# Performance work log

Hardware: AMD Instinct MI355X
Metric: run time of the kernel (lower is better)

The kernel has to match this reference:

```python
import jax, jax.numpy as jnp
import numpy as np


def _conv(x, w, b, pad):
    y = jax.lax.conv_general_dilated(x, w, (1, 1), [(pad, pad), (pad, pad)],
                                     dimension_numbers=('NCHW', 'OIHW', 'NCHW'))
    return y + b[None, :, None, None]


def _pool(x):
    return jax.lax.reduce_window(x, -jnp.inf, jax.lax.max, (1, 1, 2, 2), (1, 1, 2, 2), 'VALID')


def _up(x):
    return jnp.repeat(jnp.repeat(x, 2, axis=2), 2, axis=3)


def _unet(x, p):
    r = jax.nn.relu
    e1 = r(_conv(x, p['enc1_w'], p['enc1_b'], 1))                            # [B,16,H,W]
    e2 = r(_conv(_pool(e1), p['enc2_w'], p['enc2_b'], 1))                    # [B,32,H/2,W/2]
    bt = r(_conv(_pool(e2), p['bott_w'], p['bott_b'], 1))                    # [B,64,H/4,W/4]
    d2 = r(_conv(jnp.concatenate([_up(bt), e2], 1), p['dec2_w'], p['dec2_b'], 1))
    d1 = r(_conv(jnp.concatenate([_up(d2), e1], 1), p['dec1_w'], p['dec1_b'], 1))
    return _conv(d1, p['out_w'], p['out_b'], 0)                              # [B,C,H,W]


def _global_match(ref_e, cur_e):
    # FEELVOS global matching: for each current-frame pixel, distance to the
    # nearest reference-frame pixel in embedding space, mapped through
    # d = 1 - 2/(1+exp(||e_p - e_q||^2)). Monotone, so apply after the min.
    N, E, H, W = ref_e.shape
    a = ref_e.reshape(N, E, H * W).transpose(0, 2, 1)   # [N, P, E] reference pixels
    b = cur_e.reshape(N, E, H * W).transpose(0, 2, 1)   # [N, Q, E] current pixels
    d2 = (jnp.sum(a * a, -1)[:, :, None] + jnp.sum(b * b, -1)[:, None, :]
          - 2.0 * jnp.einsum('npe,nqe->npq', a, b))     # [N, P, Q]
    dmin = jnp.min(jnp.maximum(d2, 0.0), axis=1)        # [N, Q] nearest-neighbor dist^2
    return (1.0 - 2.0 * jax.nn.sigmoid(-dmin)).reshape(N, 1, H, W)


def setup_inputs() -> dict:
    key = jax.random.key(0)
    ks = jax.random.split(key, 16)
    B, C, H, W, CIN = 2, 4, 48, 48, 3

    def w(k, shape):
        fan_in = int(np.prod(shape[1:]))
        return jax.random.normal(k, shape, jnp.float32) * np.float32(1.0 / np.sqrt(fan_in))

    return {
        'x1': jax.random.uniform(ks[0], (B, C, H, W), jnp.float32),
        'x2': jax.random.uniform(ks[1], (B, C, H, W), jnp.float32),
        'x3': jax.random.normal(ks[2], (B, CIN, H, W), jnp.float32),
        'enc1_w': w(ks[3], (16, CIN, 3, 3)), 'enc1_b': jnp.zeros((16,), jnp.float32),
        'enc2_w': w(ks[4], (32, 16, 3, 3)), 'enc2_b': jnp.zeros((32,), jnp.float32),
        'bott_w': w(ks[5], (64, 32, 3, 3)), 'bott_b': jnp.zeros((64,), jnp.float32),
        'dec2_w': w(ks[6], (32, 96, 3, 3)), 'dec2_b': jnp.zeros((32,), jnp.float32),
        'dec1_w': w(ks[7], (16, 48, 3, 3)), 'dec1_b': jnp.zeros((16,), jnp.float32),
        'out_w': w(ks[8], (C, 16, 1, 1)), 'out_b': jnp.zeros((C,), jnp.float32),
        'emb_w': w(ks[9], (100, 1, 3, 3)), 'emb_b': jnp.zeros((100,), jnp.float32),
        'dsh_w': w(ks[10], (1, C + 3, 3, 3)), 'dsh_b': jnp.zeros((1,), jnp.float32),
    }


def reference(x1, x2, x3, enc1_w, enc1_b, enc2_w, enc2_b, bott_w, bott_b,
              dec2_w, dec2_b, dec1_w, dec1_b, out_w, out_b, emb_w, emb_b,
              dsh_w, dsh_b):
    p = dict(enc1_w=enc1_w, enc1_b=enc1_b, enc2_w=enc2_w, enc2_b=enc2_b,
             bott_w=bott_w, bott_b=bott_b, dec2_w=dec2_w, dec2_b=dec2_b,
             dec1_w=dec1_w, dec1_b=dec1_b, out_w=out_w, out_b=out_b)
    B, C, H, W = x1.shape
    x3s = _unet(x3, p)                        # backbone on current frame -> [B,C,H,W]
    # fold the per-class Python loop into the batch axis (shared weights)
    x1f = x1.reshape(B * C, 1, H, W)
    x2f = x2.reshape(B * C, 1, H, W)
    x3f = x3s.reshape(B * C, 1, H, W)
    e1 = _conv(x1f, emb_w, emb_b, 1)          # [B*C,100,H,W]
    e2 = _conv(x2f, emb_w, emb_b, 1)
    e3 = _conv(x3f, emb_w, emb_b, 1)
    gm = _global_match(e1, e3)                # first-frame matching  [B*C,1,H,W]
    lm = _global_match(e2, e3)                # previous-frame matching
    x3rep = jnp.broadcast_to(x3s[:, None], (B, C, C, H, W)).reshape(B * C, C, H, W)
    x_t = jnp.concatenate([x3rep, gm, lm, x2f], axis=1)   # [B*C, C+3, H, W]
    logits = _conv(x_t, dsh_w, dsh_b, 1).reshape(B, C, H, W)
    # faithful to the original final loop: output is cat(logits[C-2], logits[C-1])
    return jnp.concatenate([logits[:, C - 2:C - 1], logits[:, C - 1:C]], axis=1)
```

## Files before the change

kernel.cpp:

```cpp
#include <hip/hip_runtime.h>
#include <math.h>

#define THREADS 256
#define HW 2304

typedef __attribute__((ext_vector_type(8))) short short8;
typedef __attribute__((ext_vector_type(4))) float f32x4;
typedef __attribute__((ext_vector_type(8))) unsigned short us8;

typedef const __attribute__((address_space(1))) void* gas_p;
typedef __attribute__((address_space(3))) void* las_p;

__device__ __forceinline__ void gll16(const void* g, const void* l) {
    __builtin_amdgcn_global_load_lds((gas_p)g, (las_p)l, 16, 0, 0);
}

__device__ __forceinline__ void stage_rows(const float* __restrict__ src, float* __restrict__ dst,
                                           int nch, int chStride, int H, int W,
                                           int rlo, int rcount, int tid, int nthr, bool relu) {
    int rowfl = W + 4;
    int total = nch * rcount * rowfl;
    float4 z = make_float4(0.f, 0.f, 0.f, 0.f);
    for (int i = tid; i * 4 < total; i += nthr) ((float4*)dst)[i] = z;
    __syncthreads();
    int w2 = W >> 1;
    int m = nch * rcount * w2;
    for (int i = tid; i < m; i += nthr) {
        int c2 = i % w2;
        int rr = (i / w2) % rcount;
        int ch = i / (w2 * rcount);
        int srow = rlo + rr;
        if (srow < 0 || srow >= H) continue;
        float2 v = *(const float2*)(src + (size_t)ch * chStride + srow * W + 2 * c2);
        if (relu) { v.x = fmaxf(v.x, 0.f); v.y = fmaxf(v.y, 0.f); }
        *(float2*)(dst + (size_t)ch * rcount * rowfl + rr * rowfl + 2 + 2 * c2) = v;
    }
    __syncthreads();
}

#define LOAD_W9(wlbase, ci)                                        \
    const float4* wp4 = (const float4*)((wlbase) + (ci) * 12);     \
    float4 wa = wp4[0], wb = wp4[1], wc = wp4[2];                  \
    const float w9[9] = {wa.x, wa.y, wa.z, wa.w, wb.x, wb.y, wb.z, wb.w, wc.x};

__device__ __forceinline__ void emb_body(const float* __restrict__ src, int arr, int ni, int pt,
                                         const float* __restrict__ ew, const float* __restrict__ eb,
                                         unsigned short* __restrict__ hl, float* __restrict__ nrm,
                                         float* wl, int tid, int nthr) {
    for (int i = tid; i < 900; i += nthr) wl[(i / 9) * 12 + (i % 9)] = ew[i];
    for (int i = tid; i < 100; i += nthr) wl[1200 + i] = eb[i];
    __syncthreads();

    int pix = pt * 256 + tid;
    int x = pix % 48, y = pix / 48;
    float p9[9];
    #pragma unroll
    for (int ky = 0; ky < 3; ++ky)
        #pragma unroll
        for (int kx = 0; kx < 3; ++kx) {
            int yy = y + ky - 1, xx = x + kx - 1;
            p9[ky * 3 + kx] = (yy >= 0 && yy < 48 && xx >= 0 && xx < 48) ? src[yy * 48 + xx] : 0.f;
        }

    float nsum = 0.f;
    char* rowp = (char*)(hl + (((size_t)(arr * 4 + ni)) * HW + pix) * 256);
    for (int g = 0; g < 16; ++g) {
        us8 vh, vl;
        #pragma unroll
        for (int j = 0; j < 8; ++j) {
            int e = g * 8 + j;
            float v = 0.f;
            if (e < 100) {
                v = wl[1200 + e];
                #pragma unroll
                for (int k = 0; k < 9; ++k) v = fmaf(p9[k], wl[e * 12 + k], v);
                nsum = fmaf(v, v, nsum);
            }
            unsigned bits = __float_as_uint(v);
            vh[j] = (unsigned short)(bits >> 16);
            float lo = v - __uint_as_float(bits & 0xFFFF0000u);
            vl[j] = (unsigned short)(__float_as_uint(lo) >> 16);
        }
        *(us8*)(rowp + g * 16) = vh;
        *(us8*)(rowp + 256 + g * 16) = vl;
    }
    nrm[(size_t)(arr * 4 + ni) * HW + pix] = nsum;
}

__global__ __launch_bounds__(256) void k_pre(
        float* __restrict__ d2b, float* __restrict__ d1b,
        const float* __restrict__ b2, const float* __restrict__ b1,
        const float* __restrict__ x1, const float* __restrict__ x2,
        const float* __restrict__ ew, const float* __restrict__ eb,
        unsigned short* __restrict__ hl, float* __restrict__ nrm,
        unsigned* __restrict__ initbuf,
        const float* __restrict__ x3, const float* __restrict__ e1w,
        const float* __restrict__ e1b, float* __restrict__ e1u, float* __restrict__ p1) {
    __shared__ __align__(16) float lds[3 * 50 * 52];
    __shared__ __align__(16) float wl1[48];
    __shared__ float wl[1300];
    int bx = blockIdx.x;
    int tid = threadIdx.x;
    if (bx < 432) {
        int idx = bx * 256 + tid;
        if (idx < 36864) d2b[idx] = b2[(idx / 576) & 31];
        else d1b[idx - 36864] = b1[((idx - 36864) / HW) & 15];
        return;
    }
    if (bx < 504) {
        int sub = bx - 432;
        int arr = sub / 36;
        int ni = (sub % 36) / 9, pt = sub % 9;
        int plane = 2 + (ni & 1) + 4 * (ni >> 1);
        const float* src = (arr == 0 ? x1 : x2) + (size_t)plane * HW;
        emb_body(src, arr, ni, pt, ew, eb, hl, nrm, wl, tid, 256);
        return;
    }
    if (bx < 576) {
        int i = (bx - 504) * 256 + tid;
        initbuf[i] = 0x7F800000u;
        return;
    }
    int co = (bx - 576) & 15, n = (bx - 576) >> 4;
    for (int i = tid; i < 27; i += 256) wl1[(i / 9) * 12 + (i % 9)] = e1w[(co * 3) * 9 + i];
    stage_rows(x3 + (size_t)n * 3 * HW, lds, 3, HW, 48, 48, -1, 50, tid, 256, false);
    float bv = e1b[co];
    for (int o = 0; o < 3; ++o) {
        int po = o * 256 + tid;
        if (po >= 576) break;
        int py = po / 24, px = po % 24;
        float s[2][2] = {{bv, bv}, {bv, bv}};
        for (int ci = 0; ci < 3; ++ci) {
            const float* chp = lds + ci * 2600;
            float c[4][6];
            #pragma unroll
            for (int rr = 0; rr < 4; ++rr) {
                const float2* pr = (const float2*)(chp + (2 * py + rr) * 52);
                #pragma unroll
                for (int k = 0; k < 3; ++k) { float2 t = pr[px + k]; c[rr][2 * k] = t.x; c[rr][2 * k + 1] = t.y; }
            }
            LOAD_W9(wl1, ci)
            #pragma unroll
            for (int dy = 0; dy < 3; ++dy)
                #pragma unroll
                for (int dx = 0; dx < 3; ++dx) {
                    float wv = w9[dy * 3 + dx];
                    #pragma unroll
                    for (int yy = 0; yy < 2; ++yy)
                        #pragma unroll
                        for (int xx = 0; xx < 2; ++xx)
                            s[yy][xx] = fmaf(c[yy + dy][xx + dx + 1], wv, s[yy][xx]);
                }
        }
        float* ob = e1u + (size_t)(n * 16 + co) * HW;
        float mx = -INFINITY;
        #pragma unroll
        for (int yy = 0; yy < 2; ++yy)
            #pragma unroll
            for (int xx = 0; xx < 2; ++xx) {
                float v = fmaxf(s[yy][xx], 0.f);
                ob[(2 * py + yy) * 48 + 2 * px + xx] = v;
                mx = fmaxf(mx, v);
            }
        p1[(size_t)(n * 16 + co) * 576 + py * 24 + px] = mx;
    }
}

__global__ __launch_bounds__(192) void k_enc2pool(const float* __restrict__ p1, const float* __restrict__ w,
                                                  const float* __restrict__ b, float* __restrict__ e2,
                                                  float* __restrict__ p2) {
    int co = blockIdx.x & 31, n = blockIdx.x >> 5;
    int tid = threadIdx.x;
    __shared__ __align__(16) float lds[16 * 26 * 28];
    __shared__ __align__(16) float wl[192];
    for (int i = tid; i < 144; i += 192) wl[(i / 9) * 12 + (i % 9)] = w[(co * 16) * 9 + i];
    stage_rows(p1 + (size_t)n * 16 * 576, lds, 16, 576, 24, 24, -1, 26, tid, 192, false);
    if (tid < 144) {
        int py = tid / 12, px = tid % 12;
        float bv = b[co];
        float s[2][2] = {{bv, bv}, {bv, bv}};
        for (int ci = 0; ci < 16; ++ci) {
            const float* chp = lds + ci * 728;
            float c[4][6];
            #pragma unroll
            for (int rr = 0; rr < 4; ++rr) {
                const float2* pr = (const float2*)(chp + (2 * py + rr) * 28);
                #pragma unroll
                for (int k = 0; k < 3; ++k) { float2 t = pr[px + k]; c[rr][2 * k] = t.x; c[rr][2 * k + 1] = t.y; }
            }
            LOAD_W9(wl, ci)
            #pragma unroll
            for (int dy = 0; dy < 3; ++dy)
                #pragma unroll
                for (int dx = 0; dx < 3; ++dx) {
                    float wv = w9[dy * 3 + dx];
                    #pragma unroll
                    for (int yy = 0; yy < 2; ++yy)
                        #pragma unroll
                        for (int xx = 0; xx < 2; ++xx)
                            s[yy][xx] = fmaf(c[yy + dy][xx + dx + 1], wv, s[yy][xx]);
                }
        }
        float* ob = e2 + (size_t)(n * 32 + co) * 576;
        float mx = -INFINITY;
        #pragma unroll
        for (int yy = 0; yy < 2; ++yy)
            #pragma unroll
            for (int xx = 0; xx < 2; ++xx) {
                float v = fmaxf(s[yy][xx], 0.f);
                ob[(2 * py + yy) * 24 + 2 * px + xx] = v;
                mx = fmaxf(mx, v);
            }
        p2[(size_t)(n * 32 + co) * 144 + py * 12 + px] = mx;
    }
}

__global__ __launch_bounds__(192) void k_bott(const float* __restrict__ p2, const float* __restrict__ w,
                                              const float* __restrict__ b, float* __restrict__ bt) {
    int co = blockIdx.x & 63, n = blockIdx.x >> 6;
    int tid = threadIdx.x;
    __shared__ __align__(16) float lds[32 * 14 * 16];
    __shared__ __align__(16) float wl[384];
    for (int i = tid; i < 288; i += 192) wl[(i / 9) * 12 + (i % 9)] = w[(co * 32) * 9 + i];
    stage_rows(p2 + (size_t)n * 32 * 144, lds, 32, 144, 12, 12, -1, 14, tid, 192, false);
    if (tid < 144) {
        int y = tid / 12, x = tid % 12;
        float acc = b[co];
        for (int ci = 0; ci < 32; ++ci) {
            const float* chp = lds + ci * 224;
            LOAD_W9(wl, ci)
            #pragma unroll
            for (int dy = 0; dy < 3; ++dy)
                #pragma unroll
                for (int dx = 0; dx < 3; ++dx)
                    acc = fmaf(chp[(y + dy) * 16 + x + dx + 1], w9[dy * 3 + dx], acc);
        }
        bt[(size_t)(n * 64 + co) * 144 + y * 12 + x] = fmaxf(acc, 0.f);
    }
}

__global__ __launch_bounds__(192) void k_dec2p(const float* __restrict__ bt, const float* __restrict__ e2,
                                               const float* __restrict__ w, float* __restrict__ d2b) {
    int bx = blockIdx.x;
    int chunk = bx & 3, co = (bx >> 2) & 31, n = bx >> 7;
    int cib = chunk * 24;
    int nA = max(0, min(24, 64 - cib));
    int nB = 24 - nA;
    int tid = threadIdx.x;
    __shared__ __align__(16) float lds[24 * 26 * 28];
    __shared__ __align__(16) float wl[288];
    for (int i = tid; i < 216; i += 192) wl[(i / 9) * 12 + (i % 9)] = w[((size_t)co * 96 + cib) * 9 + i];
    stage_rows(bt + ((size_t)n * 64 + cib) * 144, lds, nA, 144, 12, 12, -1, 14, tid, 192, false);
    float* ldsB = lds + nA * 224;
    int e2c = max(0, cib + nA - 64);
    stage_rows(e2 + ((size_t)n * 32 + e2c) * 576, ldsB, nB, 576, 24, 24, -1, 26, tid, 192, false);
    if (tid < 144) {
        int y = tid / 6, qx = tid % 6;
        float acc[4] = {0.f, 0.f, 0.f, 0.f};
        int r0 = ((y - 1) >> 1) + 1;
        int yodd = y & 1;
        for (int ci = 0; ci < nA; ++ci) {
            const float* chp = lds + ci * 224;
            const float2* p0 = (const float2*)(chp + r0 * 16);
            const float2* p1 = (const float2*)(chp + (r0 + 1) * 16);
            float a0[6], a1[6], am[6];
            #pragma unroll
            for (int k = 0; k < 3; ++k) {
                float2 t0 = p0[qx + k], t1 = p1[qx + k];
                a0[2 * k] = t0.x; a0[2 * k + 1] = t0.y;
                a1[2 * k] = t1.x; a1[2 * k + 1] = t1.y;
            }
            #pragma unroll
            for (int k = 0; k < 6; ++k) am[k] = yodd ? a0[k] : a1[k];
            LOAD_W9(wl, ci)
            #pragma unroll
            for (int dy = 0; dy < 3; ++dy) {
                const float* rr = (dy == 0) ? a0 : (dy == 1 ? am : a1);
                #pragma unroll
                for (int dx = 0; dx < 3; ++dx) {
                    float wv = w9[dy * 3 + dx];
                    #pragma unroll
                    for (int j = 0; j < 4; ++j)
                        acc[j] = fmaf(rr[((j + dx - 1) >> 1) + 2], wv, acc[j]);
                }
            }
        }
        for (int ci = 0; ci < nB; ++ci) {
            const float* chp = ldsB + ci * 728;
            float bvv[3][8];
            #pragma unroll
            for (int r = 0; r < 3; ++r) {
                const float2* pr = (const float2*)(chp + (y + r) * 28);
                #pragma unroll
                for (int k = 0; k < 4; ++k) { float2 t = pr[2 * qx + k]; bvv[r][2 * k] = t.x; bvv[r][2 * k + 1] = t.y; }
            }
            LOAD_W9(wl, nA + ci)
            #pragma unroll
            for (int dy = 0; dy < 3; ++dy)
                #pragma unroll
                for (int dx = 0; dx < 3; ++dx) {
                    float wv = w9[dy * 3 + dx];
                    #pragma unroll
                    for (int j = 0; j < 4; ++j)
                        acc[j] = fmaf(bvv[dy][j + dx + 1], wv, acc[j]);
                }
        }
        float* op = d2b + ((size_t)(n * 32 + co)) * 576 + y * 24 + qx * 4;
        #pragma unroll
        for (int j = 0; j < 4; ++j) atomicAdd(op + j, acc[j]);
    }
}

__global__ __launch_bounds__(192) void k_dec1p(const float* __restrict__ d2b, const float* __restrict__ e1u,
                                               const float* __restrict__ w, float* __restrict__ d1b) {
    int bx = blockIdx.x;
    int strip = bx % 3;
    int chunk = (bx / 3) & 3;
    int co = (bx / 12) & 15;
    int n = bx / 192;
    int cib = chunk * 12;
    int nA = max(0, min(12, 32 - cib));
    int nB = 12 - nA;
    int y0 = strip * 16;
    int yhlo = (y0 - 1) >> 1;
    int tid = threadIdx.x;
    __shared__ __align__(16) float lds[12 * 18 * 52];
    __shared__ __align__(16) float wl[144];
    for (int i = tid; i < 108; i += 192) wl[(i / 9) * 12 + (i % 9)] = w[((size_t)co * 48 + cib) * 9 + i];
    stage_rows(d2b + ((size_t)n * 32 + cib) * 576, lds, nA, 576, 24, 24, yhlo, 10, tid, 192, true);
    float* ldsB = lds + nA * 280;
    int e1c = max(0, cib + nA - 32);
    stage_rows(e1u + ((size_t)n * 16 + e1c) * HW, ldsB, nB, HW, 48, 48, y0 - 1, 18, tid, 192, false);
    {
        int yl = tid / 12, qx = tid % 12;
        int y = y0 + yl;
        float acc[4] = {0.f, 0.f, 0.f, 0.f};
        int r0 = ((y - 1) >> 1) - yhlo;
        int yodd = y & 1;
        for (int ci = 0; ci < nA; ++ci) {
            const float* chp = lds + ci * 280;
            const float2* p0 = (const float2*)(chp + r0 * 28);
            const float2* p1 = (const float2*)(chp + (r0 + 1) * 28);
            float a0[6], a1[6], am[6];
            #pragma unroll
            for (int k = 0; k < 3; ++k) {
                float2 t0 = p0[qx + k], t1 = p1[qx + k];
                a0[2 * k] = t0.x; a0[2 * k + 1] = t0.y;
                a1[2 * k] = t1.x; a1[2 * k + 1] = t1.y;
            }
            #pragma unroll
            for (int k = 0; k < 6; ++k) am[k] = yodd ? a0[k] : a1[k];
            LOAD_W9(wl, ci)
            #pragma unroll
            for (int dy = 0; dy < 3; ++dy) {
                const float* rr = (dy == 0) ? a0 : (dy == 1 ? am : a1);
                #pragma unroll
                for (int dx = 0; dx < 3; ++dx) {
                    float wv = w9[dy * 3 + dx];
                    #pragma unroll
                    for (int j = 0; j < 4; ++j)
                        acc[j] = fmaf(rr[((j + dx - 1) >> 1) + 2], wv, acc[j]);
                }
            }
        }
        for (int ci = 0; ci < nB; ++ci) {
            const float* chp = ldsB + ci * 936;
            float bvv[3][8];
            #pragma unroll
            for (int r = 0; r < 3; ++r) {
                const float2* pr = (const float2*)(chp + (yl + r) * 52);
                #pragma unroll
                for (int k = 0; k < 4; ++k) { float2 t = pr[2 * qx + k]; bvv[r][2 * k] = t.x; bvv[r][2 * k + 1] = t.y; }
            }
            LOAD_W9(wl, nA + ci)
            #pragma unroll
            for (int dy = 0; dy < 3; ++dy)
                #pragma unroll
                for (int dx = 0; dx < 3; ++dx) {
                    float wv = w9[dy * 3 + dx];
                    #pragma unroll
                    for (int j = 0; j < 4; ++j)
                        acc[j] = fmaf(bvv[dy][j + dx + 1], wv, acc[j]);
                }
        }
        float* op = d1b + ((size_t)(n * 16 + co)) * HW + y * 48 + qx * 4;
        #pragma unroll
        for (int j = 0; j < 4; ++j) atomicAdd(op + j, acc[j]);
    }
}

__global__ void k_out1x1(const float* __restrict__ d1b, const float* __restrict__ ow,
                         const float* __restrict__ ob, float* __restrict__ x3s) {
    int idx = blockIdx.x * THREADS + threadIdx.x;
    if (idx >= 18432) return;
    int q = idx % HW;
    int co = (idx / HW) & 3;
    int n = idx / 9216;
    float acc = ob[co];
    #pragma unroll
    for (int ci = 0; ci < 16; ++ci)
        acc = fmaf(fmaxf(d1b[((size_t)(n * 16 + ci)) * HW + q], 0.f), ow[co * 16 + ci], acc);
    x3s[((size_t)(n * 4 + co)) * HW + q] = acc;
}

__global__ __launch_bounds__(256) void k_emb3(const float* __restrict__ x3s,
                                              const float* __restrict__ ew, const float* __restrict__ eb,
                                              unsigned short* __restrict__ hl, float* __restrict__ nrm) {
    __shared__ float wl[1300];
    int ni = blockIdx.x / 9, pt = blockIdx.x % 9;
    int plane = 2 + (ni & 1) + 4 * (ni >> 1);
    emb_body(x3s + (size_t)plane * HW, 2, ni, pt, ew, eb, hl, nrm, wl, threadIdx.x, 256);
}

#define NPC 24
__global__ __launch_bounds__(256, 2) void k_match(
        const unsigned short* __restrict__ hl, const float* __restrict__ nrm,
        unsigned* __restrict__ gmd, unsigned* __restrict__ lmd) {
    int bx = blockIdx.x;
    int l = (bx & 7) * 54 + (bx >> 3);
    int ps = l % 3;
    int qt = (l / 3) % 18;
    int mn = l / 54;
    int n = mn & 3;
    int m = mn >> 2;

    const unsigned short* curhl = hl + ((size_t)(8 + n)) * HW * 256;
    const unsigned short* refhl = hl + ((size_t)(m * 4 + n)) * HW * 256;
    const float* na = nrm + (size_t)(m * 4 + n) * HW;
    const float* nb = nrm + (size_t)(8 + n) * HW;
    unsigned* outd = (m == 0 ? gmd : lmd) + (size_t)n * HW;

    int qbase = qt * 128;
    int pbase = ps * 768;

    __shared__ __align__(16) unsigned short refl[2][32 * 256];
    __shared__ __align__(16) float nal[768];

    int tid = threadIdx.x;
    int wave = tid >> 6;
    int lane = tid & 63;
    int lr = lane >> 5;
    int lc = lane & 31;

    if (tid < 192) *(float4*)&nal[tid * 4] = *(const float4*)(na + pbase + tid * 4);

    short8 ahi[2][4], alo[2][4];
    #pragma unroll
    for (int j = 0; j < 2; ++j) {
        int r = qbase + wave * 32 + j * 16 + (lane & 15);
        const unsigned short* rp = curhl + (size_t)r * 256;
        #pragma unroll
        for (int ks = 0; ks < 4; ++ks) {
            const unsigned short* p = rp + (ks * 4 + (lane >> 4)) * 8;
            ahi[j][ks] = *(const short8*)p;
            alo[j][ks] = *(const short8*)(p + 128);
        }
    }

    {
        const unsigned short* gb = refhl + (size_t)pbase * 256;
        #pragma unroll
        for (int t = 0; t < 4; ++t) {
            int i = wave * 4 + t;
            int r = 2 * i + lr;
            gll16(gb + (size_t)r * 256 + (lc ^ (r & 7)) * 8, &refl[0][i * 512]);
        }
    }
    asm volatile("s_waitcnt lgkmcnt(0)" ::: "memory");

    float dmin[2][4];
    #pragma unroll
    for (int j = 0; j < 2; ++j)
        #pragma unroll
        for (int r = 0; r < 4; ++r) dmin[j][r] = INFINITY;

    for (int pc = 0; pc < NPC; ++pc) {
        int cur = pc & 1;
        if (pc + 1 < NPC) {
            const unsigned short* gb = refhl + (size_t)(pbase + (pc + 1) * 32) * 256;
            #pragma unroll
            for (int t = 0; t < 4; ++t) {
                int i = wave * 4 + t;
                int r = 2 * i + lr;
                gll16(gb + (size_t)r * 256 + (lc ^ (r & 7)) * 8, &refl[cur ^ 1][i * 512]);
            }
            asm volatile("s_waitcnt vmcnt(4)" ::: "memory");
        } else {
            asm volatile("s_waitcnt vmcnt(0)" ::: "memory");
        }
        __builtin_amdgcn_s_barrier();

        short8 bhi[2][4], blo[2][4];
        #pragma unroll
        for (int ptile = 0; ptile < 2; ++ptile) {
            int r = ptile * 16 + (lane & 15);
            #pragma unroll
            for (int ks = 0; ks < 4; ++ks) {
                int cg = ks * 4 + (lane >> 4);
                const char* p = (const char*)refl[cur] + r * 512 + ((cg ^ (r & 7)) << 4);
                bhi[ptile][ks] = *(const short8*)p;
                blo[ptile][ks] = *(const short8*)(p + 256);
            }
        }

        f32x4 acc[2][2];
        #pragma unroll
        for (int ptile = 0; ptile < 2; ++ptile)
            #pragma unroll
            for (int j = 0; j < 2; ++j) acc[ptile][j] = (f32x4){0.f, 0.f, 0.f, 0.f};

        #pragma unroll
        for (int ks = 0; ks < 4; ++ks) {
            #pragma unroll
            for (int ptile = 0; ptile < 2; ++ptile)
                #pragma unroll
                for (int j = 0; j < 2; ++j)
                    acc[ptile][j] = __builtin_amdgcn_mfma_f32_16x16x32_bf16(
                        ahi[j][ks], bhi[ptile][ks], acc[ptile][j], 0, 0, 0);
            #pragma unroll
            for (int ptile = 0; ptile < 2; ++ptile)
                #pragma unroll
                for (int j = 0; j < 2; ++j)
                    acc[ptile][j] = __builtin_amdgcn_mfma_f32_16x16x32_bf16(
                        ahi[j][ks], blo[ptile][ks], acc[ptile][j], 0, 0, 0);
            #pragma unroll
            for (int ptile = 0; ptile < 2; ++ptile)
                #pragma unroll
                for (int j = 0; j < 2; ++j)
                    acc[ptile][j] = __builtin_amdgcn_mfma_f32_16x16x32_bf16(
                        alo[j][ks], bhi[ptile][ks], acc[ptile][j], 0, 0, 0);
        }

        #pragma unroll
        for (int ptile = 0; ptile < 2; ++ptile) {
            float nav = nal[pc * 32 + ptile * 16 + (lane & 15)];
            #pragma unroll
            for (int j = 0; j < 2; ++j)
                #pragma unroll
                for (int r = 0; r < 4; ++r)
                    dmin[j][r] = fminf(dmin[j][r], fmaf(-2.f, acc[ptile][j][r], nav));
        }
        __builtin_amdgcn_s_barrier();
    }

    #pragma unroll
    for (int j = 0; j < 2; ++j)
        #pragma unroll
        for (int r = 0; r < 4; ++r) {
            float v = dmin[j][r];
            v = fminf(v, __shfl_xor(v, 1, 64));
            v = fminf(v, __shfl_xor(v, 2, 64));
            v = fminf(v, __shfl_xor(v, 4, 64));
            v = fminf(v, __shfl_xor(v, 8, 64));
            if ((lane & 15) == 0) {
                int q = qbase + wave * 32 + j * 16 + 4 * (lane >> 4) + r;
                float d2 = fmaxf(v + nb[q], 0.f);
                atomicMin(&outd[q], __float_as_uint(d2));
            }
        }
}

__global__ void k_final(const float* __restrict__ x3s, const unsigned* __restrict__ gmd,
                        const unsigned* __restrict__ lmd, const float* __restrict__ x2,
                        const float* __restrict__ dshw, const float* __restrict__ dshb,
                        float* __restrict__ out) {
    int idx = blockIdx.x * THREADS + threadIdx.x;
    if (idx >= 9216) return;
    int q = idx % HW, ni = idx / HW;
    int n = 2 + (ni & 1) + 4 * (ni >> 1);
    int b = ni >> 1;
    int x = q % 48, y = q / 48;
    float acc = dshb[0];
    for (int c = 0; c < 7; ++c) {
        const float* wp = dshw + c * 9;
        #pragma unroll
        for (int ky = 0; ky < 3; ++ky) {
            int yy = y + ky - 1;
            if (yy < 0 || yy >= 48) continue;
            #pragma unroll
            for (int kx = 0; kx < 3; ++kx) {
                int xx = x + kx - 1;
                if (xx < 0 || xx >= 48) continue;
                float v;
                if (c < 4) v = x3s[(size_t)(b * 4 + c) * HW + yy * 48 + xx];
                else if (c == 4) {
                    float d2 = __uint_as_float(gmd[(size_t)ni * HW + yy * 48 + xx]);
                    v = 1.f - 2.f / (1.f + expf(d2));
                } else if (c == 5) {
                    float d2 = __uint_as_float(lmd[(size_t)ni * HW + yy * 48 + xx]);
                    v = 1.f - 2.f / (1.f + expf(d2));
                } else v = x2[(size_t)n * HW + yy * 48 + xx];
                acc = fmaf(v, wp[ky * 3 + kx], acc);
            }
        }
    }
    out[idx] = acc;
}

extern "C" void kernel_launch(void* const* d_in, const int* in_sizes, int n_in,
                              void* d_out, int out_size, void* d_ws, size_t ws_size,
                              hipStream_t stream) {
    const float* x1     = (const float*)d_in[0];
    const float* x2     = (const float*)d_in[1];
    const float* x3     = (const float*)d_in[2];
    const float* enc1_w = (const float*)d_in[3];
    const float* enc1_b = (const float*)d_in[4];
    const float* enc2_w = (const float*)d_in[5];
    const float* enc2_b = (const float*)d_in[6];
    const float* bott_w = (const float*)d_in[7];
    const float* bott_b = (const float*)d_in[8];
    const float* dec2_w = (const float*)d_in[9];
    const float* dec2_b = (const float*)d_in[10];
    const float* dec1_w = (const float*)d_in[11];
    const float* dec1_b = (const float*)d_in[12];
    const float* out_w  = (const float*)d_in[13];
    const float* out_b  = (const float*)d_in[14];
    const float* emb_w  = (const float*)d_in[15];
    const float* emb_b  = (const float*)d_in[16];
    const float* dsh_w  = (const float*)d_in[17];
    const float* dsh_b  = (const float*)d_in[18];

    float* w = (float*)d_ws;
    float* e1u  = w;
    float* p1   = w + 73728;
    float* e2   = w + 92160;
    float* p2   = w + 129024;
    float* bt   = w + 138240;
    float* d2b  = w + 156672;
    float* d1b  = w + 193536;
    float* x3s  = w + 267264;
    float* nrm  = w + 285696;
    unsigned* gmd = (unsigned*)(w + 313344);
    unsigned* lmd = (unsigned*)(w + 322560);
    unsigned short* hl = (unsigned short*)(w + 331776);

    k_pre<<<dim3(608), dim3(256), 0, stream>>>(d2b, d1b, dec2_b, dec1_b, x1, x2, emb_w, emb_b,
                                               hl, nrm, gmd, x3, enc1_w, enc1_b, e1u, p1);
    k_enc2pool<<<dim3(64), dim3(192), 0, stream>>>(p1, enc2_w, enc2_b, e2, p2);
    k_bott<<<dim3(128), dim3(192), 0, stream>>>(p2, bott_w, bott_b, bt);
    k_dec2p<<<dim3(256), dim3(192), 0, stream>>>(bt, e2, dec2_w, d2b);
    k_dec1p<<<dim3(384), dim3(192), 0, stream>>>(d2b, e1u, dec1_w, d1b);
    k_out1x1<<<dim3(72), dim3(THREADS), 0, stream>>>(d1b, out_w, out_b, x3s);
    k_emb3<<<dim3(36), dim3(256), 0, stream>>>(x3s, emb_w, emb_b, hl, nrm);
    k_match<<<dim3(432), dim3(256), 0, stream>>>(hl, nrm, gmd, lmd);
    k_final<<<dim3(36), dim3(THREADS), 0, stream>>>(x3s, gmd, lmd, x2, dsh_w, dsh_b, (float*)d_out);
}
```

Before: 136.8 us.

## Fuse out1x1 into emb3 and spread reference embeddings across UNet kernels

The 1x1 output conv is fused into the current-frame embedding kernel, which recomputes the needed x3s taps from d1b directly, removing one launch. Extra blocks in the same kernel still write x3s for the final stage. The x1 and x2 reference embeddings move out of k_pre into spare blocks of the enc2 and bottleneck kernels, so they fill otherwise idle CUs in those small-grid stages. Bias and init fills are vectorised to float4/uint4, and the enc2 and bott kernels now run 256 threads with a shared LDS buffer. The cost is redundant 1x1 recomputation (9 taps x 16 channels per pixel) and more LDS per block in the enc2 and bott kernels.

```diff
diff --git a/kernel.cpp b/kernel.cpp
--- a/kernel.cpp
+++ b/kernel.cpp
@@ -43,6 +43,34 @@
     float4 wa = wp4[0], wb = wp4[1], wc = wp4[2];                  \
     const float w9[9] = {wa.x, wa.y, wa.z, wa.w, wb.x, wb.y, wb.z, wb.w, wc.x};
 
+__device__ __forceinline__ void emb_tail(const float* p9, int arr, int ni, int pix,
+                                         unsigned short* __restrict__ hl, float* __restrict__ nrm,
+                                         const float* wl) {
+    float nsum = 0.f;
+    char* rowp = (char*)(hl + (((size_t)(arr * 4 + ni)) * HW + pix) * 256);
+    for (int g = 0; g < 16; ++g) {
+        us8 vh, vl;
+        #pragma unroll
+        for (int j = 0; j < 8; ++j) {
+            int e = g * 8 + j;
+            float v = 0.f;
+            if (e < 100) {
+                v = wl[1200 + e];
+                #pragma unroll
+                for (int k = 0; k < 9; ++k) v = fmaf(p9[k], wl[e * 12 + k], v);
+                nsum = fmaf(v, v, nsum);
+            }
+            unsigned bits = __float_as_uint(v);
+            vh[j] = (unsigned short)(bits >> 16);
+            float lo = v - __uint_as_float(bits & 0xFFFF0000u);
+            vl[j] = (unsigned short)(__float_as_uint(lo) >> 16);
+        }
+        *(us8*)(rowp + g * 16) = vh;
+        *(us8*)(rowp + 256 + g * 16) = vl;
+    }
+    nrm[(size_t)(arr * 4 + ni) * HW + pix] = nsum;
+}
+
 __device__ __forceinline__ void emb_body(const float* __restrict__ src, int arr, int ni, int pt,
                                          const float* __restrict__ ew, const float* __restrict__ eb,
                                          unsigned short* __restrict__ hl, float* __restrict__ nrm,
@@ -61,67 +89,32 @@
             int yy = y + ky - 1, xx = x + kx - 1;
             p9[ky * 3 + kx] = (yy >= 0 && yy < 48 && xx >= 0 && xx < 48) ? src[yy * 48 + xx] : 0.f;
         }
-
-    float nsum = 0.f;
-    char* rowp = (char*)(hl + (((size_t)(arr * 4 + ni)) * HW + pix) * 256);
-    for (int g = 0; g < 16; ++g) {
-        us8 vh, vl;
-        #pragma unroll
-        for (int j = 0; j < 8; ++j) {
-            int e = g * 8 + j;
-            float v = 0.f;
-            if (e < 100) {
-                v = wl[1200 + e];
-                #pragma unroll
-                for (int k = 0; k < 9; ++k) v = fmaf(p9[k], wl[e * 12 + k], v);
-                nsum = fmaf(v, v, nsum);
-            }
-            unsigned bits = __float_as_uint(v);
-            vh[j] = (unsigned short)(bits >> 16);
-            float lo = v - __uint_as_float(bits & 0xFFFF0000u);
-            vl[j] = (unsigned short)(__float_as_uint(lo) >> 16);
-        }
-        *(us8*)(rowp + g * 16) = vh;
-        *(us8*)(rowp + 256 + g * 16) = vl;
-    }
-    nrm[(size_t)(arr * 4 + ni) * HW + pix] = nsum;
+    emb_tail(p9, arr, ni, pix, hl, nrm, wl);
 }
 
 __global__ __launch_bounds__(256) void k_pre(
         float* __restrict__ d2b, float* __restrict__ d1b,
         const float* __restrict__ b2, const float* __restrict__ b1,
-        const float* __restrict__ x1, const float* __restrict__ x2,
-        const float* __restrict__ ew, const float* __restrict__ eb,
-        unsigned short* __restrict__ hl, float* __restrict__ nrm,
         unsigned* __restrict__ initbuf,
         const float* __restrict__ x3, const float* __restrict__ e1w,
         const float* __restrict__ e1b, float* __restrict__ e1u, float* __restrict__ p1) {
     __shared__ __align__(16) float lds[3 * 50 * 52];
     __shared__ __align__(16) float wl1[48];
-    __shared__ float wl[1300];
     int bx = blockIdx.x;
     int tid = threadIdx.x;
-    if (bx < 432) {
-        int idx = bx * 256 + tid;
-        if (idx < 36864) d2b[idx] = b2[(idx / 576) & 31];
-        else d1b[idx - 36864] = b1[((idx - 36864) / HW) & 15];
+    if (bx < 108) {
+        int i4 = bx * 256 + tid;
+        if (i4 < 9216) { int ch = (i4 / 144) & 31; float v = b2[ch]; ((float4*)d2b)[i4] = make_float4(v, v, v, v); }
+        else { int j = i4 - 9216; int ch = (j / 576) & 15; float v = b1[ch]; ((float4*)d1b)[j] = make_float4(v, v, v, v); }
         return;
     }
-    if (bx < 504) {
-        int sub = bx - 432;
-        int arr = sub / 36;
-        int ni = (sub % 36) / 9, pt = sub % 9;
-        int plane = 2 + (ni & 1) + 4 * (ni >> 1);
-        const float* src = (arr == 0 ? x1 : x2) + (size_t)plane * HW;
-        emb_body(src, arr, ni, pt, ew, eb, hl, nrm, wl, tid, 256);
+    if (bx < 126) {
+        int i = (bx - 108) * 256 + tid;
+        uint4 f; f.x = f.y = f.z = f.w = 0x7F800000u;
+        ((uint4*)initbuf)[i] = f;
         return;
     }
-    if (bx < 576) {
-        int i = (bx - 504) * 256 + tid;
-        initbuf[i] = 0x7F800000u;
-        return;
-    }
-    int co = (bx - 576) & 15, n = (bx - 576) >> 4;
+    int co = (bx - 126) & 15, n = (bx - 126) >> 4;
     for (int i = tid; i < 27; i += 256) wl1[(i / 9) * 12 + (i % 9)] = e1w[(co * 3) * 9 + i];
     stage_rows(x3 + (size_t)n * 3 * HW, lds, 3, HW, 48, 48, -1, 50, tid, 256, false);
     float bv = e1b[co];
@@ -166,15 +159,26 @@
     }
 }
 
-__global__ __launch_bounds__(192) void k_enc2pool(const float* __restrict__ p1, const float* __restrict__ w,
+__global__ __launch_bounds__(256) void k_enc2pool(const float* __restrict__ p1, const float* __restrict__ w,
                                                   const float* __restrict__ b, float* __restrict__ e2,
-                                                  float* __restrict__ p2) {
+                                                  float* __restrict__ p2,
+                                                  const float* __restrict__ x1, const float* __restrict__ ew,
+                                                  const float* __restrict__ eb,
+                                                  unsigned short* __restrict__ hl, float* __restrict__ nrm) {
+    __shared__ __align__(16) float smem[11840];
+    int tid = threadIdx.x;
+    if (blockIdx.x >= 64) {
+        int sub = blockIdx.x - 64;
+        int ni = sub / 9, pt = sub % 9;
+        int plane = 2 + (ni & 1) + 4 * (ni >> 1);
+        emb_body(x1 + (size_t)plane * HW, 0, ni, pt, ew, eb, hl, nrm, smem, tid, 256);
+        return;
+    }
     int co = blockIdx.x & 31, n = blockIdx.x >> 5;
-    int tid = threadIdx.x;
-    __shared__ __align__(16) float lds[16 * 26 * 28];
-    __shared__ __align__(16) float wl[192];
-    for (int i = tid; i < 144; i += 192) wl[(i / 9) * 12 + (i % 9)] = w[(co * 16) * 9 + i];
-    stage_rows(p1 + (size_t)n * 16 * 576, lds, 16, 576, 24, 24, -1, 26, tid, 192, false);
+    float* lds = smem;
+    float* wl = smem + 11648;
+    for (int i = tid; i < 144; i += 256) wl[(i / 9) * 12 + (i % 9)] = w[(co * 16) * 9 + i];
+    stage_rows(p1 + (size_t)n * 16 * 576, lds, 16, 576, 24, 24, -1, 26, tid, 256, false);
     if (tid < 144) {
         int py = tid / 12, px = tid % 12;
         float bv = b[co];
@@ -215,14 +219,25 @@
     }
 }
 
-__global__ __launch_bounds__(192) void k_bott(const float* __restrict__ p2, const float* __restrict__ w,
-                                              const float* __restrict__ b, float* __restrict__ bt) {
+__global__ __launch_bounds__(256) void k_bott(const float* __restrict__ p2, const float* __restrict__ w,
+                                              const float* __restrict__ b, float* __restrict__ bt,
+                                              const float* __restrict__ x2, const float* __restrict__ ew,
+                                              const float* __restrict__ eb,
+                                              unsigned short* __restrict__ hl, float* __restrict__ nrm) {
+    __shared__ __align__(16) float smem[7552];
+    int tid = threadIdx.x;
+    if (blockIdx.x >= 128) {
+        int sub = blockIdx.x - 128;
+        int ni = sub / 9, pt = sub % 9;
+        int plane = 2 + (ni & 1) + 4 * (ni >> 1);
+        emb_body(x2 + (size_t)plane * HW, 1, ni, pt, ew, eb, hl, nrm, smem, tid, 256);
+        return;
+    }
     int co = blockIdx.x & 63, n = blockIdx.x >> 6;
-    int tid = threadIdx.x;
-    __shared__ __align__(16) float lds[32 * 14 * 16];
-    __shared__ __align__(16) float wl[384];
-    for (int i = tid; i < 288; i += 192) wl[(i / 9) * 12 + (i % 9)] = w[(co * 32) * 9 + i];
-    stage_rows(p2 + (size_t)n * 32 * 144, lds, 32, 144, 12, 12, -1, 14, tid, 192, false);
+    float* lds = smem;
+    float* wl = smem + 7168;
+    for (int i = tid; i < 288; i += 256) wl[(i / 9) * 12 + (i % 9)] = w[(co * 32) * 9 + i];
+    stage_rows(p2 + (size_t)n * 32 * 144, lds, 32, 144, 12, 12, -1, 14, tid, 256, false);
     if (tid < 144) {
         int y = tid / 12, x = tid % 12;
         float acc = b[co];
@@ -389,27 +404,56 @@
     }
 }
 
-__global__ void k_out1x1(const float* __restrict__ d1b, const float* __restrict__ ow,
-                         const float* __restrict__ ob, float* __restrict__ x3s) {
-    int idx = blockIdx.x * THREADS + threadIdx.x;
-    if (idx >= 18432) return;
-    int q = idx % HW;
-    int co = (idx / HW) & 3;
-    int n = idx / 9216;
-    float acc = ob[co];
+__global__ __launch_bounds__(256) void k_embout(const float* __restrict__ d1b,
+                                                const float* __restrict__ ow, const float* __restrict__ obias,
+                                                const float* __restrict__ ew, const float* __restrict__ eb,
+                                                unsigned short* __restrict__ hl, float* __restrict__ nrm,
+                                                float* __restrict__ x3s) {
+    __shared__ float wl[1300];
+    int tid = threadIdx.x;
+    if (blockIdx.x >= 36) {
+        int idx = (blockIdx.x - 36) * 256 + tid;
+        int q = idx % HW;
+        int co = (idx / HW) & 3;
+        int n = idx / 9216;
+        float acc = obias[co];
+        #pragma unroll
+        for (int ci = 0; ci < 16; ++ci)
+            acc = fmaf(fmaxf(d1b[((size_t)(n * 16 + ci)) * HW + q], 0.f), ow[co * 16 + ci], acc);
+        x3s[((size_t)(n * 4 + co)) * HW + q] = acc;
+        return;
+    }
+    int ni = blockIdx.x / 9, pt = blockIdx.x % 9;
+    int n = ni >> 1, co = 2 + (ni & 1);
+    for (int i = tid; i < 900; i += 256) wl[(i / 9) * 12 + (i % 9)] = ew[i];
+    for (int i = tid; i < 100; i += 256) wl[1200 + i] = eb[i];
+    __syncthreads();
+
+    float owr[16];
     #pragma unroll
-    for (int ci = 0; ci < 16; ++ci)
-        acc = fmaf(fmaxf(d1b[((size_t)(n * 16 + ci)) * HW + q], 0.f), ow[co * 16 + ci], acc);
-    x3s[((size_t)(n * 4 + co)) * HW + q] = acc;
-}
-
-__global__ __launch_bounds__(256) void k_emb3(const float* __restrict__ x3s,
-                                              const float* __restrict__ ew, const float* __restrict__ eb,
-                                              unsigned short* __restrict__ hl, float* __restrict__ nrm) {
-    __shared__ float wl[1300];
-    int ni = blockIdx.x / 9, pt = blockIdx.x % 9;
-    int plane = 2 + (ni & 1) + 4 * (ni >> 1);
-    emb_body(x3s + (size_t)plane * HW, 2, ni, pt, ew, eb, hl, nrm, wl, threadIdx.x, 256);
+    for (int k = 0; k < 16; ++k) owr[k] = ow[co * 16 + k];
+    float ob = obias[co];
+    const float* dp = d1b + (size_t)n * 16 * HW;
+
+    int pix = pt * 256 + tid;
+    int x = pix % 48, y = pix / 48;
+    float p9[9];
+    #pragma unroll
+    for (int ky = 0; ky < 3; ++ky)
+        #pragma unroll
+        for (int kx = 0; kx < 3; ++kx) {
+            int yy = y + ky - 1, xx = x + kx - 1;
+            float v = 0.f;
+            if (yy >= 0 && yy < 48 && xx >= 0 && xx < 48) {
+                v = ob;
+                int off = yy * 48 + xx;
+                #pragma unroll
+                for (int ci = 0; ci < 16; ++ci)
+                    v = fmaf(fmaxf(dp[(size_t)ci * HW + off], 0.f), owr[ci], v);
+            }
+            p9[ky * 3 + kx] = v;
+        }
+    emb_tail(p9, 2, ni, pix, hl, nrm, wl);
 }
 
 #define NPC 24
@@ -634,14 +678,15 @@
     unsigned* lmd = (unsigned*)(w + 322560);
     unsigned short* hl = (unsigned short*)(w + 331776);
 
-    k_pre<<<dim3(608), dim3(256), 0, stream>>>(d2b, d1b, dec2_b, dec1_b, x1, x2, emb_w, emb_b,
-                                               hl, nrm, gmd, x3, enc1_w, enc1_b, e1u, p1);
-    k_enc2pool<<<dim3(64), dim3(192), 0, stream>>>(p1, enc2_w, enc2_b, e2, p2);
-    k_bott<<<dim3(128), dim3(192), 0, stream>>>(p2, bott_w, bott_b, bt);
+    k_pre<<<dim3(158), dim3(256), 0, stream>>>(d2b, d1b, dec2_b, dec1_b, gmd,
+                                               x3, enc1_w, enc1_b, e1u, p1);
+    k_enc2pool<<<dim3(100), dim3(256), 0, stream>>>(p1, enc2_w, enc2_b, e2, p2,
+                                                    x1, emb_w, emb_b, hl, nrm);
+    k_bott<<<dim3(164), dim3(256), 0, stream>>>(p2, bott_w, bott_b, bt,
+                                                x2, emb_w, emb_b, hl, nrm);
     k_dec2p<<<dim3(256), dim3(192), 0, stream>>>(bt, e2, dec2_w, d2b);
     k_dec1p<<<dim3(384), dim3(192), 0, stream>>>(d2b, e1u, dec1_w, d1b);
-    k_out1x1<<<dim3(72), dim3(THREADS), 0, stream>>>(d1b, out_w, out_b, x3s);
-    k_emb3<<<dim3(36), dim3(256), 0, stream>>>(x3s, emb_w, emb_b, hl, nrm);
+    k_embout<<<dim3(108), dim3(256), 0, stream>>>(d1b, out_w, out_b, emb_w, emb_b, hl, nrm, x3s);
     k_match<<<dim3(432), dim3(256), 0, stream>>>(hl, nrm, gmd, lmd);
     k_final<<<dim3(36), dim3(THREADS), 0, stream>>>(x3s, gmd, lmd, x2, dsh_w, dsh_b, (float*)d_out);
 }
```

After: 139.2 us. No clear change (+1.7%).

## Fuse out1x1 conv and current-frame embedding into the matching kernel

Applied to the files above, without the earlier changes.

Removes the separate out1x1 and emb3 launches. Each matching block now recomputes the current-frame embedding for its 128 query pixels in registers, from a relu'd d1b tile staged in shared memory, and keeps the query norms in LDS. 72 extra blocks in the same launch write x3s for the final kernel. This saves two launches and the global round trip of the current embedding, in exchange for redundant embedding work, since each query tile is recomputed by 6 blocks, and larger LDS use that may lower occupancy.

```diff
diff --git a/kernel.cpp b/kernel.cpp
--- a/kernel.cpp
+++ b/kernel.cpp
@@ -389,33 +389,27 @@
     }
 }
 
-__global__ void k_out1x1(const float* __restrict__ d1b, const float* __restrict__ ow,
-                         const float* __restrict__ ob, float* __restrict__ x3s) {
-    int idx = blockIdx.x * THREADS + threadIdx.x;
-    if (idx >= 18432) return;
-    int q = idx % HW;
-    int co = (idx / HW) & 3;
-    int n = idx / 9216;
-    float acc = ob[co];
-    #pragma unroll
-    for (int ci = 0; ci < 16; ++ci)
-        acc = fmaf(fmaxf(d1b[((size_t)(n * 16 + ci)) * HW + q], 0.f), ow[co * 16 + ci], acc);
-    x3s[((size_t)(n * 4 + co)) * HW + q] = acc;
-}
-
-__global__ __launch_bounds__(256) void k_emb3(const float* __restrict__ x3s,
-                                              const float* __restrict__ ew, const float* __restrict__ eb,
-                                              unsigned short* __restrict__ hl, float* __restrict__ nrm) {
-    __shared__ float wl[1300];
-    int ni = blockIdx.x / 9, pt = blockIdx.x % 9;
-    int plane = 2 + (ni & 1) + 4 * (ni >> 1);
-    emb_body(x3s + (size_t)plane * HW, 2, ni, pt, ew, eb, hl, nrm, wl, threadIdx.x, 256);
-}
-
 #define NPC 24
-__global__ __launch_bounds__(256, 2) void k_match(
+__global__ __launch_bounds__(256, 2) void k_matchx(
         const unsigned short* __restrict__ hl, const float* __restrict__ nrm,
-        unsigned* __restrict__ gmd, unsigned* __restrict__ lmd) {
+        const float* __restrict__ d1b, const float* __restrict__ ow,
+        const float* __restrict__ obias, const float* __restrict__ ew,
+        const float* __restrict__ eb,
+        unsigned* __restrict__ gmd, unsigned* __restrict__ lmd,
+        float* __restrict__ x3s) {
+    int tid = threadIdx.x;
+    if (blockIdx.x >= 432) {
+        int idx = (blockIdx.x - 432) * 256 + tid;
+        int q = idx % HW;
+        int co = (idx / HW) & 3;
+        int n = idx / 9216;
+        float acc = obias[co];
+        #pragma unroll
+        for (int ci = 0; ci < 16; ++ci)
+            acc = fmaf(fmaxf(d1b[((size_t)(n * 16 + ci)) * HW + q], 0.f), ow[co * 16 + ci], acc);
+        x3s[((size_t)(n * 4 + co)) * HW + q] = acc;
+        return;
+    }
     int bx = blockIdx.x;
     int l = (bx & 7) * 54 + (bx >> 3);
     int ps = l % 3;
@@ -424,38 +418,106 @@
     int n = mn & 3;
     int m = mn >> 2;
 
-    const unsigned short* curhl = hl + ((size_t)(8 + n)) * HW * 256;
     const unsigned short* refhl = hl + ((size_t)(m * 4 + n)) * HW * 256;
     const float* na = nrm + (size_t)(m * 4 + n) * HW;
-    const float* nb = nrm + (size_t)(8 + n) * HW;
     unsigned* outd = (m == 0 ? gmd : lmd) + (size_t)n * HW;
 
     int qbase = qt * 128;
     int pbase = ps * 768;
 
-    __shared__ __align__(16) unsigned short refl[2][32 * 256];
-    __shared__ __align__(16) float nal[768];
-
-    int tid = threadIdx.x;
+    __shared__ __align__(16) float smem[15296];
+    unsigned short* refl0 = (unsigned short*)smem;
+    unsigned short* refl1 = refl0 + 32 * 256;
+    float* nal = smem + 8192;
+    float* wl  = smem + 8960;
+    float* nbl = smem + 10260;
+    float* dtile = smem + 10392;
+
     int wave = tid >> 6;
     int lane = tid & 63;
     int lr = lane >> 5;
     int lc = lane & 31;
 
     if (tid < 192) *(float4*)&nal[tid * 4] = *(const float4*)(na + pbase + tid * 4);
+    for (int i = tid; i < 900; i += 256) wl[(i / 9) * 12 + (i % 9)] = ew[i];
+    for (int i = tid; i < 100; i += 256) wl[1200 + i] = eb[i];
+
+    int b_ = n >> 1;
+    int co_ = 2 + (n & 1);
+    const float* dp = d1b + (size_t)b_ * 16 * HW;
+    int y0t = qbase / 48 - 1;
+    for (int i = tid; i < 1152; i += 256) {
+        int ci = i / 72;
+        int pp = (i % 72) * 4;
+        int yy = y0t + pp / 48;
+        int xx = pp % 48;
+        float4 v = make_float4(0.f, 0.f, 0.f, 0.f);
+        if (yy >= 0 && yy < 48) {
+            v = *(const float4*)(dp + (size_t)ci * HW + yy * 48 + xx);
+            v.x = fmaxf(v.x, 0.f); v.y = fmaxf(v.y, 0.f);
+            v.z = fmaxf(v.z, 0.f); v.w = fmaxf(v.w, 0.f);
+        }
+        dtile[(pp + 0) * 17 + ci] = v.x;
+        dtile[(pp + 1) * 17 + ci] = v.y;
+        dtile[(pp + 2) * 17 + ci] = v.z;
+        dtile[(pp + 3) * 17 + ci] = v.w;
+    }
+    __syncthreads();
+
+    float owr[16];
+    #pragma unroll
+    for (int k = 0; k < 16; ++k) owr[k] = ow[co_ * 16 + k];
+    float obv = obias[co_];
 
     short8 ahi[2][4], alo[2][4];
+    int eb0 = (lane >> 4) * 8;
     #pragma unroll
     for (int j = 0; j < 2; ++j) {
-        int r = qbase + wave * 32 + j * 16 + (lane & 15);
-        const unsigned short* rp = curhl + (size_t)r * 256;
+        int rloc = wave * 32 + j * 16 + (lane & 15);
+        int r = qbase + rloc;
+        int x = r % 48, y = r / 48;
+        float p9[9];
+        #pragma unroll
+        for (int ky = 0; ky < 3; ++ky)
+            #pragma unroll
+            for (int kx = 0; kx < 3; ++kx) {
+                int yy = y + ky - 1, xx = x + kx - 1;
+                float v = 0.f;
+                if (yy >= 0 && yy < 48 && xx >= 0 && xx < 48) {
+                    v = obv;
+                    const float* dpix = &dtile[((yy - y0t) * 48 + xx) * 17];
+                    #pragma unroll
+                    for (int ci = 0; ci < 16; ++ci) v = fmaf(dpix[ci], owr[ci], v);
+                }
+                p9[ky * 3 + kx] = v;
+            }
+        float nsum = 0.f;
         #pragma unroll
         for (int ks = 0; ks < 4; ++ks) {
-            const unsigned short* p = rp + (ks * 4 + (lane >> 4)) * 8;
-            ahi[j][ks] = *(const short8*)p;
-            alo[j][ks] = *(const short8*)(p + 128);
-        }
-    }
+            short8 vh, vlo;
+            #pragma unroll
+            for (int t = 0; t < 8; ++t) {
+                int e = ks * 32 + eb0 + t;
+                float v = 0.f;
+                if (e < 100) {
+                    v = wl[1200 + e];
+                    #pragma unroll
+                    for (int k = 0; k < 9; ++k) v = fmaf(p9[k], wl[e * 12 + k], v);
+                    nsum = fmaf(v, v, nsum);
+                }
+                unsigned bits = __float_as_uint(v);
+                vh[t] = (short)(bits >> 16);
+                float lo = v - __uint_as_float(bits & 0xFFFF0000u);
+                vlo[t] = (short)(__float_as_uint(lo) >> 16);
+            }
+            ahi[j][ks] = vh;
+            alo[j][ks] = vlo;
+        }
+        nsum += __shfl_xor(nsum, 16, 64);
+        nsum += __shfl_xor(nsum, 32, 64);
+        if ((lane >> 4) == 0) nbl[rloc] = nsum;
+    }
+    __syncthreads();
 
     {
         const unsigned short* gb = refhl + (size_t)pbase * 256;
@@ -463,7 +525,7 @@
         for (int t = 0; t < 4; ++t) {
             int i = wave * 4 + t;
             int r = 2 * i + lr;
-            gll16(gb + (size_t)r * 256 + (lc ^ (r & 7)) * 8, &refl[0][i * 512]);
+            gll16(gb + (size_t)r * 256 + (lc ^ (r & 7)) * 8, refl0 + i * 512);
         }
     }
     asm volatile("s_waitcnt lgkmcnt(0)" ::: "memory");
@@ -475,14 +537,15 @@
         for (int r = 0; r < 4; ++r) dmin[j][r] = INFINITY;
 
     for (int pc = 0; pc < NPC; ++pc) {
-        int cur = pc & 1;
+        unsigned short* cur = (pc & 1) ? refl1 : refl0;
+        unsigned short* nxt = (pc & 1) ? refl0 : refl1;
         if (pc + 1 < NPC) {
             const unsigned short* gb = refhl + (size_t)(pbase + (pc + 1) * 32) * 256;
             #pragma unroll
             for (int t = 0; t < 4; ++t) {
                 int i = wave * 4 + t;
                 int r = 2 * i + lr;
-                gll16(gb + (size_t)r * 256 + (lc ^ (r & 7)) * 8, &refl[cur ^ 1][i * 512]);
+                gll16(gb + (size_t)r * 256 + (lc ^ (r & 7)) * 8, nxt + i * 512);
             }
             asm volatile("s_waitcnt vmcnt(4)" ::: "memory");
         } else {
@@ -497,7 +560,7 @@
             #pragma unroll
             for (int ks = 0; ks < 4; ++ks) {
                 int cg = ks * 4 + (lane >> 4);
-                const char* p = (const char*)refl[cur] + r * 512 + ((cg ^ (r & 7)) << 4);
+                const char* p = (const char*)cur + r * 512 + ((cg ^ (r & 7)) << 4);
                 bhi[ptile][ks] = *(const short8*)p;
                 blo[ptile][ks] = *(const short8*)(p + 256);
             }
@@ -553,9 +616,9 @@
             v = fminf(v, __shfl_xor(v, 4, 64));
             v = fminf(v, __shfl_xor(v, 8, 64));
             if ((lane & 15) == 0) {
-                int q = qbase + wave * 32 + j * 16 + 4 * (lane >> 4) + r;
-                float d2 = fmaxf(v + nb[q], 0.f);
-                atomicMin(&outd[q], __float_as_uint(d2));
+                int qloc = wave * 32 + j * 16 + 4 * (lane >> 4) + r;
+                float d2 = fmaxf(v + nbl[qloc], 0.f);
+                atomicMin(&outd[qbase + qloc], __float_as_uint(d2));
             }
         }
 }
@@ -640,8 +703,7 @@
     k_bott<<<dim3(128), dim3(192), 0, stream>>>(p2, bott_w, bott_b, bt);
     k_dec2p<<<dim3(256), dim3(192), 0, stream>>>(bt, e2, dec2_w, d2b);
     k_dec1p<<<dim3(384), dim3(192), 0, stream>>>(d2b, e1u, dec1_w, d1b);
-    k_out1x1<<<dim3(72), dim3(THREADS), 0, stream>>>(d1b, out_w, out_b, x3s);
-    k_emb3<<<dim3(36), dim3(256), 0, stream>>>(x3s, emb_w, emb_b, hl, nrm);
-    k_match<<<dim3(432), dim3(256), 0, stream>>>(hl, nrm, gmd, lmd);
+    k_matchx<<<dim3(504), dim3(256), 0, stream>>>(hl, nrm, d1b, out_w, out_b, emb_w, emb_b,
+                                                  gmd, lmd, x3s);
     k_final<<<dim3(36), dim3(THREADS), 0, stream>>>(x3s, gmd, lmd, x2, dsh_w, dsh_b, (float*)d_out);
 }
```

After: 125.2 us. 8.5% less time.
